# Kernel tuning notes

Hardware: AMD Instinct MI355X
Metric: run time of the kernel (lower is better)

## Reference

```python
import jax, jax.numpy as jnp
import numpy as np
import math

L = 8           # n_layers
DIM = 1024
H = 16          # num_heads
HD = DIM // H   # head_dim
HID = 4096      # mlp hidden
V = 32000       # vocab
B, T = 2, 1024


def setup_inputs() -> dict:
    key = jax.random.key(0)
    ks = jax.random.split(key, 10)
    s = 0.02
    inp = {
        "input_ids": jax.random.randint(ks[0], (B, T), 0, V, dtype=jnp.int32),
        "labels": jax.random.randint(ks[1], (B, T), 0, V, dtype=jnp.int32),
        "Wemb": jax.random.normal(ks[2], (V, DIM), jnp.float32) * s,   # tied embed / lm_head
        "Wq": jax.random.normal(ks[3], (L, DIM, DIM), jnp.float32) * s,
        "Wk": jax.random.normal(ks[4], (L, DIM, DIM), jnp.float32) * s,
        "Wv": jax.random.normal(ks[5], (L, DIM, DIM), jnp.float32) * s,
        "Wo": jax.random.normal(ks[6], (L, DIM, DIM), jnp.float32) * s,
        "Wfc": jax.random.normal(ks[7], (L, DIM, HID), jnp.float32) * s,
        "Wgate": jax.random.normal(ks[8], (L, DIM, HID), jnp.float32) * s,
        "Wproj": jax.random.normal(ks[9], (L, HID, DIM), jnp.float32) * s,
    }
    return inp


def _forward(input_ids, labels, Wemb, Wq, Wk, Wv, Wo, Wfc, Wgate, Wproj):
    b, t = input_ids.shape
    h = Wemb[input_ids]                                   # [B,T,C] embedding lookup
    # causal additive mask: -inf strictly above diagonal
    mask = jnp.triu(jnp.full((t, t), -jnp.inf, dtype=h.dtype), k=1)
    inv_sqrt_L = 1.0 / math.sqrt(L)
    inv_sqrt_hd = 1.0 / math.sqrt(HD)
    inv_sqrt_hid = 1.0 / math.sqrt(HID)

    def block(h, params):
        wq, wk, wv, wo, wfc, wgate, wproj = params
        # attention (explicit QK^T softmax V, as in source)
        q = (h @ wq).reshape(b, t, H, HD)
        k = (h @ wk).reshape(b, t, H, HD)
        v = (h @ wv).reshape(b, t, H, HD)
        scores = jnp.einsum("bqhd,bkhd->bhqk", q, k) * inv_sqrt_hd + mask
        probs = jax.nn.softmax(scores, axis=-1)
        attn = jnp.einsum("bhqk,bkhd->bqhd", probs, v).reshape(b, t, DIM)
        h = h + (attn @ wo) * inv_sqrt_L
        # SwiGLU MLP with 1/sqrt(hidden) scaling
        mlp = (((h @ wfc) * jax.nn.silu(h @ wgate)) * inv_sqrt_hid) @ wproj
        h = h + mlp * inv_sqrt_L
        return h, None

    h, _ = jax.lax.scan(block, h, (Wq, Wk, Wv, Wo, Wfc, Wgate, Wproj))

    logits = h @ Wemb.T                                   # tied lm_head [B,T,V]
    # cross entropy with ignore_index=-1
    lab = labels.reshape(-1)
    valid = lab != -1
    safe = jnp.where(valid, lab, 0)
    logp = jax.nn.log_softmax(logits.reshape(-1, V), axis=-1)
    nll = -jnp.take_along_axis(logp, safe[:, None], axis=-1)[:, 0]
    loss = jnp.sum(jnp.where(valid, nll, 0.0)) / jnp.maximum(jnp.sum(valid), 1)
    return logits, loss


def reference(input_ids, labels, Wemb, Wq, Wk, Wv, Wo, Wfc, Wgate, Wproj):
    return _forward(input_ids, labels, Wemb, Wq, Wk, Wv, Wo, Wfc, Wgate, Wproj)
```

## Files before the change

kernel.cpp:

```cpp
#include <hip/hip_runtime.h>
#include <hip/hip_bf16.h>
#include <math.h>

#define L_LAYERS 8
#define DIM 1024
#define NH 16
#define HD 64
#define HID 4096
#define VOCAB 32000
#define BB 2
#define TT 1024
#define MROWS (BB*TT)

typedef unsigned short u16;
typedef short short8 __attribute__((ext_vector_type(8)));
typedef float f32x4 __attribute__((ext_vector_type(4)));
typedef unsigned short us4 __attribute__((ext_vector_type(4)));
typedef unsigned short us8 __attribute__((ext_vector_type(8)));

__device__ __forceinline__ float bf2f(u16 x){
  union { unsigned int u; float f; } v; v.u = ((unsigned int)x) << 16; return v.f;
}
__device__ __forceinline__ u16 f2bf(float f){
  union { float f; unsigned int u; } v; v.f = f;
  unsigned int r = (v.u + 0x7fffu + ((v.u >> 16) & 1u)) >> 16; return (u16)r;
}

#define AS1 __attribute__((address_space(1)))
#define AS3 __attribute__((address_space(3)))
__device__ __forceinline__ void gld_lds16(const void* g, void* l){
  __builtin_amdgcn_global_load_lds((const AS1 void*)g, (AS3 void*)l, 16, 0, 0);
}

__global__ void k_embed(const int* __restrict__ ids, const float* __restrict__ Wemb,
                        float* __restrict__ h, u16* __restrict__ hb){
  int bt = blockIdx.x; long id = ids[bt];
  const float4* src = (const float4*)(Wemb + id*(long)DIM);
  float4 v = src[threadIdx.x];
  ((float4*)(h + (long)bt*DIM))[threadIdx.x] = v;
  us4 o = { f2bf(v.x), f2bf(v.y), f2bf(v.z), f2bf(v.w) };
  ((us4*)(hb + (long)bt*DIM))[threadIdx.x] = o;
}

__global__ void k_cvt(const float* __restrict__ src, u16* __restrict__ dst, long n){
  long i = ((long)blockIdx.x*256 + threadIdx.x)*8;
  if (i >= n) return;
  float4 a = ((const float4*)(src+i))[0];
  float4 b = ((const float4*)(src+i))[1];
  us4 o0 = { f2bf(a.x), f2bf(a.y), f2bf(a.z), f2bf(a.w) };
  us4 o1 = { f2bf(b.x), f2bf(b.y), f2bf(b.z), f2bf(b.w) };
  ((us4*)(dst+i))[0] = o0; ((us4*)(dst+i))[1] = o1;
}

__global__ void k_cvt_layer(const float* __restrict__ Wq, const float* __restrict__ Wk,
    const float* __restrict__ Wv, const float* __restrict__ Wo,
    const float* __restrict__ Wfc, const float* __restrict__ Wg, const float* __restrict__ Wp,
    u16* __restrict__ qkvT, u16* __restrict__ woT, u16* __restrict__ fgT, u16* __restrict__ projT)
{
  int tile = blockIdx.x;
  const float* src; u16* dst; int R, C, tr, tc;
  long rowmul = 1, rowoff = 0;
  if (tile < 1024){
    int m = tile >> 8, t2 = tile & 255;
    tr = t2 >> 4; tc = t2 & 15; R = 1024; C = 1024;
    src = (m==0)?Wq:(m==1)?Wk:(m==2)?Wv:Wo;
    dst = (m<3)? qkvT + (long)m*1024*1024 : woT;
  } else if (tile < 3072){
    int m = (tile - 1024) >> 10, t2 = (tile - 1024) & 1023;
    tr = t2 >> 6; tc = t2 & 63; R = 1024; C = 4096;
    src = m ? Wg : Wfc; dst = fgT; rowmul = 2; rowoff = m;
  } else {
    int t2 = tile - 3072;
    tr = t2 >> 4; tc = t2 & 15; R = 4096; C = 1024;
    src = Wp; dst = projT;
  }
  __shared__ float ls[64][65];
  int u = threadIdx.x, rr = u & 63, cc = u >> 6;
  const float* sp = src + (long)(tr*64 + rr)*C + tc*64 + cc*16;
  float4 v0 = ((const float4*)sp)[0];
  float4 v1 = ((const float4*)sp)[1];
  float4 v2 = ((const float4*)sp)[2];
  float4 v3 = ((const float4*)sp)[3];
  ls[rr][cc*16+ 0]=v0.x; ls[rr][cc*16+ 1]=v0.y; ls[rr][cc*16+ 2]=v0.z; ls[rr][cc*16+ 3]=v0.w;
  ls[rr][cc*16+ 4]=v1.x; ls[rr][cc*16+ 5]=v1.y; ls[rr][cc*16+ 6]=v1.z; ls[rr][cc*16+ 7]=v1.w;
  ls[rr][cc*16+ 8]=v2.x; ls[rr][cc*16+ 9]=v2.y; ls[rr][cc*16+10]=v2.z; ls[rr][cc*16+11]=v2.w;
  ls[rr][cc*16+12]=v3.x; ls[rr][cc*16+13]=v3.y; ls[rr][cc*16+14]=v3.z; ls[rr][cc*16+15]=v3.w;
  __syncthreads();
  int d  = u >> 2;
  int c4 = u & 3;
  long drow = (long)tc*64 + d;
  u16* dp = dst + (drow*rowmul + rowoff)*R + tr*64;
  #pragma unroll
  for (int g2 = 0; g2 < 2; ++g2){
    int e0 = (c4 + g2*4) * 8;
    us8 o;
    #pragma unroll
    for (int j=0;j<8;j++) o[j] = f2bf(ls[e0+j][d]);
    *((us8*)(dp + e0)) = o;
  }
}

template<int EPI>
__global__ __launch_bounds__(256, 2) void k_gemm(
    const u16* __restrict__ A, long lda,
    const u16* __restrict__ Bt, long ldb,
    void* __restrict__ Cp, long ldc,
    int K, int nMt, float alpha, int ksplit,
    u16* __restrict__ hbout)
{
  __shared__ u16 lsA[128*32];
  __shared__ u16 lsB[128*32];
  int nflat = gridDim.x; int w = blockIdx.x;
  if ((nflat & 7) == 0){ int q = nflat >> 3; w = (w & 7)*q + (w >> 3); }
  int perk = nflat / ksplit;
  int kc = w / perk; int w2 = w - kc*perk;
  int mtile = w2 % nMt, ntile = w2 / nMt;
  const u16* Ab = A + (long)mtile*128*lda + (long)kc*K;
  const u16* Bb = Bt + (long)ntile*128*ldb + (long)kc*K;
  int t = threadIdx.x;
  int wv = t >> 6, ln = t & 63;
  int srow = t >> 2;
  int scol = (t & 3) * 8;
  int fr = ln & 15, kg = ln >> 4;
  int wr = wv >> 1, wc = wv & 1;
  const f32x4 zero = {0.f,0.f,0.f,0.f};
  f32x4 acc[4][4];
  #pragma unroll
  for (int m=0;m<4;m++)
    #pragma unroll
    for (int n=0;n<4;n++) acc[m][n] = zero;
  const u16* ga0 = Ab + (long)srow*lda + scol;
  const u16* ga1 = Ab + (long)(srow+64)*lda + scol;
  const u16* gb0 = Bb + (long)srow*ldb + scol;
  const u16* gb1 = Bb + (long)(srow+64)*ldb + scol;
  u16* la0 = lsA + wv*512;
  u16* la1 = lsA + 2048 + wv*512;
  u16* lb0 = lsB + wv*512;
  u16* lb1 = lsB + 2048 + wv*512;
  for (int k0 = 0; k0 < K; k0 += 32){
    gld_lds16(ga0 + k0, la0);
    gld_lds16(ga1 + k0, la1);
    gld_lds16(gb0 + k0, lb0);
    gld_lds16(gb1 + k0, lb1);
    __syncthreads();
    short8 af[4], bfr[4];
    #pragma unroll
    for (int m=0;m<4;m++) af[m]  = *(const short8*)(lsA + (wr*64 + m*16 + fr)*32 + kg*8);
    #pragma unroll
    for (int n=0;n<4;n++) bfr[n] = *(const short8*)(lsB + (wc*64 + n*16 + fr)*32 + kg*8);
    #pragma unroll
    for (int m=0;m<4;m++)
      #pragma unroll
      for (int n=0;n<4;n++)
        acc[m][n] = __builtin_amdgcn_mfma_f32_16x16x32_bf16(af[m], bfr[n], acc[m][n], 0, 0, 0);
    __syncthreads();
  }
  long row0 = (long)mtile*128 + wr*64 + kg*4;
  int col0 = ntile*128 + wc*64 + fr;
  if constexpr (EPI == 0){
    u16* C = (u16*)Cp;
    #pragma unroll
    for (int m=0;m<4;m++)
      #pragma unroll
      for (int r=0;r<4;r++){
        long row = row0 + m*16 + r;
        #pragma unroll
        for (int n=0;n<4;n++) C[row*ldc + col0 + n*16] = f2bf(acc[m][n][r]);
      }
  } else if constexpr (EPI == 2){
    float* C = (float*)Cp;
    #pragma unroll
    for (int m=0;m<4;m++)
      #pragma unroll
      for (int r=0;r<4;r++){
        long row = row0 + m*16 + r;
        #pragma unroll
        for (int n=0;n<4;n++){
          long idx = row*ldc + col0 + n*16;
          float v = C[idx] + acc[m][n][r]*alpha;
          C[idx] = v;
          hbout[idx] = f2bf(v);
        }
      }
  } else {
    float* C = (float*)Cp + (long)kc*MROWS*ldc;
    #pragma unroll
    for (int m=0;m<4;m++)
      #pragma unroll
      for (int r=0;r<4;r++){
        long row = row0 + m*16 + r;
        #pragma unroll
        for (int n=0;n<4;n++) C[row*ldc + col0 + n*16] = acc[m][n][r];
      }
  }
}

__global__ void k_redK(const float* __restrict__ pK, float* __restrict__ h, u16* __restrict__ hb){
  long idx = ((long)blockIdx.x*256 + threadIdx.x)*4;
  const float aL = 0.35355339059327373f;
  float4 s0 = *(const float4*)(pK + idx);
  float4 s1 = *(const float4*)(pK + idx + (long)MROWS*1024);
  float4 s2 = *(const float4*)(pK + idx + (long)2*MROWS*1024);
  float4 s3 = *(const float4*)(pK + idx + (long)3*MROWS*1024);
  float4 hv = *(const float4*)(h + idx);
  float4 v;
  v.x = hv.x + (s0.x+s1.x+s2.x+s3.x)*aL;
  v.y = hv.y + (s0.y+s1.y+s2.y+s3.y)*aL;
  v.z = hv.z + (s0.z+s1.z+s2.z+s3.z)*aL;
  v.w = hv.w + (s0.w+s1.w+s2.w+s3.w)*aL;
  *(float4*)(h + idx) = v;
  us4 o = { f2bf(v.x), f2bf(v.y), f2bf(v.z), f2bf(v.w) };
  *(us4*)(hb + idx) = o;
}

#define MFMA_(va,vb,vc) __builtin_amdgcn_mfma_f32_16x16x32_bf16(va,vb,vc,0,0,0)
#define RD(slot, row, ku) (*(const short8*)(lds + (slot)*8192 + (row)*64 + ((((ku) ^ ((row)&7)))<<3)))
#define STG(base, ld, h, k0, slot) do{ \
    int u0_ = tid, r0_ = u0_>>3, c0_ = u0_&7; \
    gld_lds16((base) + (long)((h)*128 + r0_)*(ld) + (k0) + ((c0_^(r0_&7))<<3), \
              lds + (slot)*8192 + (wid*64)*8); \
    int u1_ = 512 + tid, r1_ = u1_>>3, c1_ = u1_&7; \
    gld_lds16((base) + (long)((h)*128 + r1_)*(ld) + (k0) + ((c1_^(r1_&7))<<3), \
              lds + (slot)*8192 + (512 + wid*64)*8); \
  }while(0)
#define PHASE(sA, sB, mh, nh, SC, SBASE, SLD, SH, SKOFS, SSLOT, DOWAIT) do{ \
    short8 a00 = RD(sA, wm*64 +  0 + fr, kg); \
    short8 a01 = RD(sA, wm*64 + 16 + fr, kg); \
    short8 a02 = RD(sA, wm*64 + 32 + fr, kg); \
    short8 a03 = RD(sA, wm*64 + 48 + fr, kg); \
    short8 a10 = RD(sA, wm*64 +  0 + fr, 4+kg); \
    short8 a11 = RD(sA, wm*64 + 16 + fr, 4+kg); \
    short8 a12 = RD(sA, wm*64 + 32 + fr, 4+kg); \
    short8 a13 = RD(sA, wm*64 + 48 + fr, 4+kg); \
    short8 b00 = RD(sB, wn*32 +  0 + fr, kg); \
    short8 b01 = RD(sB, wn*32 + 16 + fr, kg); \
    short8 b10 = RD(sB, wn*32 +  0 + fr, 4+kg); \
    short8 b11 = RD(sB, wn*32 + 16 + fr, 4+kg); \
    if (SC) STG(SBASE, SLD, SH, SKOFS, SSLOT); \
    if (DOWAIT){ \
      if (SC) asm volatile("s_waitcnt vmcnt(4)" ::: "memory"); \
      else    asm volatile("s_waitcnt vmcnt(0)" ::: "memory"); \
    } \
    asm volatile("s_barrier" ::: "memory"); \
    __builtin_amdgcn_s_setprio(1); \
    acc[(mh)*4+0][(nh)*2+0] = MFMA_(a00,b00,acc[(mh)*4+0][(nh)*2+0]); \
    acc[(mh)*4+1][(nh)*2+0] = MFMA_(a01,b00,acc[(mh)*4+1][(nh)*2+0]); \
    acc[(mh)*4+2][(nh)*2+0] = MFMA_(a02,b00,acc[(mh)*4+2][(nh)*2+0]); \
    acc[(mh)*4+3][(nh)*2+0] = MFMA_(a03,b00,acc[(mh)*4+3][(nh)*2+0]); \
    acc[(mh)*4+0][(nh)*2+1] = MFMA_(a00,b01,acc[(mh)*4+0][(nh)*2+1]); \
    acc[(mh)*4+1][(nh)*2+1] = MFMA_(a01,b01,acc[(mh)*4+1][(nh)*2+1]); \
    acc[(mh)*4+2][(nh)*2+1] = MFMA_(a02,b01,acc[(mh)*4+2][(nh)*2+1]); \
    acc[(mh)*4+3][(nh)*2+1] = MFMA_(a03,b01,acc[(mh)*4+3][(nh)*2+1]); \
    acc[(mh)*4+0][(nh)*2+0] = MFMA_(a10,b10,acc[(mh)*4+0][(nh)*2+0]); \
    acc[(mh)*4+1][(nh)*2+0] = MFMA_(a11,b10,acc[(mh)*4+1][(nh)*2+0]); \
    acc[(mh)*4+2][(nh)*2+0] = MFMA_(a12,b10,acc[(mh)*4+2][(nh)*2+0]); \
    acc[(mh)*4+3][(nh)*2+0] = MFMA_(a13,b10,acc[(mh)*4+3][(nh)*2+0]); \
    acc[(mh)*4+0][(nh)*2+1] = MFMA_(a10,b11,acc[(mh)*4+0][(nh)*2+1]); \
    acc[(mh)*4+1][(nh)*2+1] = MFMA_(a11,b11,acc[(mh)*4+1][(nh)*2+1]); \
    acc[(mh)*4+2][(nh)*2+1] = MFMA_(a12,b11,acc[(mh)*4+2][(nh)*2+1]); \
    acc[(mh)*4+3][(nh)*2+1] = MFMA_(a13,b11,acc[(mh)*4+3][(nh)*2+1]); \
    __builtin_amdgcn_s_setprio(0); \
    asm volatile("s_barrier" ::: "memory"); \
  }while(0)

template<int EPI>
__global__ __launch_bounds__(512, 1) void k_gemm256(
    const u16* __restrict__ A, long lda,
    const u16* __restrict__ Bt, long ldb,
    void* __restrict__ Cp, long ldc,
    int K, int nMt,
    float2* __restrict__ partials)
{
  __shared__ u16 lds[65536];
  int nwg = gridDim.x; int w = blockIdx.x;
  { int q = nwg >> 3, r8 = nwg & 7; int xcd = w & 7, lw = w >> 3;
    w = (xcd < r8 ? xcd*(q+1) : r8*(q+1) + (xcd-r8)*q) + lw; }
  int mtile = w % nMt, ntile = w / nMt;
  const u16* Abase = A + (long)mtile*256*lda;
  const u16* Bbase = Bt + (long)ntile*256*ldb;
  int tid = threadIdx.x;
  int wid = tid >> 6, ln = tid & 63;
  int wm = wid >> 2, wn = wid & 3;
  int fr = ln & 15, kg = ln >> 4;

  f32x4 acc[8][4];
  #pragma unroll
  for (int a=0;a<8;a++)
    #pragma unroll
    for (int b=0;b<4;b++) acc[a][b] = (f32x4){0.f,0.f,0.f,0.f};

  const int NT = K >> 6;
  STG(Abase, lda, 0, 0, 0);
  STG(Bbase, ldb, 0, 0, 2);
  STG(Abase, lda, 1, 0, 1);
  STG(Bbase, ldb, 1, 0, 3);
  if (NT > 1){
    STG(Abase, lda, 0, 64, 4);
    STG(Bbase, ldb, 1, 64, 7);
    asm volatile("s_waitcnt vmcnt(4)" ::: "memory");
  } else {
    asm volatile("s_waitcnt vmcnt(0)" ::: "memory");
  }
  asm volatile("s_barrier" ::: "memory");

  for (int jt = 0; jt < NT; jt += 2){
    {
      long k1 = ((long)jt+1)<<6, k2 = ((long)jt+2)<<6;
      bool s1 = (jt+1 < NT), s2 = (jt+2 < NT);
      PHASE(0,2,0,0, s1, Abase, lda, 1, k1, 5, 0);
      PHASE(0,3,0,1, s1, Bbase, ldb, 0, k1, 6, 0);
      PHASE(1,3,1,1, s2, Abase, lda, 0, k2, 0, 0);
      PHASE(1,2,1,0, s2, Bbase, ldb, 1, k2, 3, 1);
    }
    if (jt+1 < NT){
      long k1 = ((long)jt+2)<<6, k2 = ((long)jt+3)<<6;
      bool s1 = (jt+2 < NT), s2 = (jt+3 < NT);
      PHASE(4,6,0,0, s1, Abase, lda, 1, k1, 1, 0);
      PHASE(4,7,0,1, s1, Bbase, ldb, 0, k1, 2, 0);
      PHASE(5,7,1,1, s2, Abase, lda, 0, k2, 4, 0);
      PHASE(5,6,1,0, s2, Bbase, ldb, 1, k2, 7, 1);
    }
  }

  if constexpr (EPI == 3){
    u16* act = (u16*)Cp;
    const float sc = 0.015625f;
    #pragma unroll
    for (int a=0;a<8;a++){
      long rowb = (long)mtile*256 + (a>>2)*128 + wm*64 + (a&3)*16 + kg*4;
      #pragma unroll
      for (int r=0;r<4;r++){
        #pragma unroll
        for (int b=0;b<4;b++){
          float v = acc[a][b][r];
          float pv = __shfl_xor(v, 1);
          if (!(fr & 1)){
            int colg = ntile*256 + (b>>1)*128 + wn*32 + (b&1)*16 + fr;
            float g = pv;
            float sl = g / (1.0f + __expf(-g));
            act[(rowb+r)*ldc + (colg>>1)] = f2bf(v * sl * sc);
          }
        }
      }
    }
  } else {
    float* C = (float*)Cp;
    #pragma unroll
    for (int a=0;a<8;a++){
      long rowb = (long)mtile*256 + (a>>2)*128 + wm*64 + (a&3)*16 + kg*4;
      #pragma unroll
      for (int r=0;r<4;r++){
        #pragma unroll
        for (int b=0;b<4;b++){
          int colg = ntile*256 + (b>>1)*128 + wn*32 + (b&1)*16 + fr;
          C[(rowb+r)*ldc + colg] = acc[a][b][r];
        }
      }
    }
    float* pm = (float*)lds;
    float* ps = pm + 1024;
    #pragma unroll
    for (int a=0;a<8;a++)
      #pragma unroll
      for (int r=0;r<4;r++){
        float M = fmaxf(fmaxf(acc[a][0][r],acc[a][1][r]), fmaxf(acc[a][2][r],acc[a][3][r]));
        #pragma unroll
        for (int o=1;o<16;o<<=1) M = fmaxf(M, __shfl_xor(M, o));
        float S = __expf(acc[a][0][r]-M) + __expf(acc[a][1][r]-M)
                + __expf(acc[a][2][r]-M) + __expf(acc[a][3][r]-M);
        #pragma unroll
        for (int o=1;o<16;o<<=1) S += __shfl_xor(S, o);
        if (fr == 0){
          int rl = (a>>2)*128 + wm*64 + (a&3)*16 + kg*4 + r;
          pm[wn*256 + rl] = M; ps[wn*256 + rl] = S;
        }
      }
    __syncthreads();
    if (tid < 256){
      float m0 = pm[tid], m1 = pm[256+tid], m2 = pm[512+tid], m3 = pm[768+tid];
      float M = fmaxf(fmaxf(m0,m1), fmaxf(m2,m3));
      float S = ps[tid]*__expf(m0-M) + ps[256+tid]*__expf(m1-M)
              + ps[512+tid]*__expf(m2-M) + ps[768+tid]*__expf(m3-M);
      partials[((long)mtile*256 + tid)*128 + ntile] = make_float2(M, S);
    }
  }
}

__global__ void k_transpose_v(const u16* __restrict__ qkv, u16* __restrict__ vT){
  int ttile = blockIdx.x; int z = blockIdx.y;
  long b = z >> 4; int hh = z & 15;
  const u16* v = qkv + b*TT*3072 + 2048 + hh*64;
  u16* outp = vT + (long)z*64*TT;
  __shared__ u16 ls[64][65];
  int u = threadIdx.x, rr = u & 63, cc = u >> 6;
  const u16* sp = v + (long)(ttile*64 + rr)*3072 + cc*16;
  us4 a0 = ((const us4*)sp)[0];
  us4 a1 = ((const us4*)sp)[1];
  us4 a2 = ((const us4*)sp)[2];
  us4 a3 = ((const us4*)sp)[3];
  #pragma unroll
  for (int j=0;j<4;j++){ ls[rr][cc*16+j] = a0[j]; ls[rr][cc*16+4+j] = a1[j];
                         ls[rr][cc*16+8+j] = a2[j]; ls[rr][cc*16+12+j] = a3[j]; }
  __syncthreads();
  int d = u & 63;
  #pragma unroll
  for (int g=0; g<4; ++g){
    int tl = cc*16 + g*4;
    int t  = ttile*64 + tl;
    int ut = (t >> 3) & 15;
    int tp = (t & ~127) + (((ut ^ (d & 15)) << 3) | (t & 7));
    us4 o = { ls[tl+0][d], ls[tl+1][d], ls[tl+2][d], ls[tl+3][d] };
    *((us4*)(outp + (long)d*TT + tp)) = o;
  }
}

__global__ __launch_bounds__(128) void k_flash(
    const u16* __restrict__ qkv, const u16* __restrict__ vT, u16* __restrict__ attnb)
{
  __shared__ u16 lsQ[64*64];
  __shared__ u16 lsK[128*64];
  __shared__ u16 lsV[64*128];
  __shared__ u16 lsP[64*128];
  int qt = blockIdx.x; int z = blockIdx.y;
  long bT = (long)(z >> 4) * TT;
  int h64 = (z & 15) * 64;
  int t = threadIdx.x, wv = t >> 6, ln = t & 63;
  int fr = ln & 15, kg = ln >> 4;
  const u16* vbase = vT + (long)z*64*TT;

  #pragma unroll
  for (int p=0; p<4; ++p){
    int r = p*16 + wv*8 + (ln>>3);
    const u16* g = qkv + (bT + qt*64 + r)*3072 + h64 + (((ln&7) ^ (ln>>3))*8);
    gld_lds16(g, lsQ + (p*16 + wv*8)*64);
  }

  f32x4 S[2][8], O[2][4];
  float Mst[2][4], Lst[2][4];
  #pragma unroll
  for (int m=0;m<2;m++){
    #pragma unroll
    for (int n=0;n<4;n++) O[m][n] = (f32x4){0.f,0.f,0.f,0.f};
    #pragma unroll
    for (int r=0;r<4;r++){ Mst[m][r] = -3.0e38f; Lst[m][r] = 0.f; }
  }

  int nk = (qt >> 1) + 1;
  for (int kt = 0; kt < nk; ++kt){
    #pragma unroll
    for (int p=0; p<8; ++p){
      int r = p*16 + wv*8 + (ln>>3);
      const u16* g = qkv + (bT + kt*128 + r)*3072 + 1024 + h64 + (((ln&7) ^ (ln>>3))*8);
      gld_lds16(g, lsK + (p*16 + wv*8)*64);
    }
    #pragma unroll
    for (int p=0; p<8; ++p){
      int d = p*8 + wv*4 + (ln>>4);
      const u16* g = vbase + (long)d*TT + kt*128 + (ln&15)*8;
      gld_lds16(g, lsV + (p*8 + wv*4)*128);
    }
    __syncthreads();

    #pragma unroll
    for (int m=0;m<2;m++)
      #pragma unroll
      for (int n=0;n<8;n++) S[m][n] = (f32x4){0.f,0.f,0.f,0.f};
    #pragma unroll
    for (int ks=0; ks<2; ++ks){
      int un = ((ks*4 + kg) ^ (fr & 7)) * 8;
      short8 a0 = *(const short8*)(lsQ + (wv*32 +      fr)*64 + un);
      short8 a1 = *(const short8*)(lsQ + (wv*32 + 16 + fr)*64 + un);
      #pragma unroll
      for (int n=0;n<8;n++){
        short8 bb = *(const short8*)(lsK + (n*16 + fr)*64 + un);
        S[0][n] = __builtin_amdgcn_mfma_f32_16x16x32_bf16(a0, bb, S[0][n], 0,0,0);
        S[1][n] = __builtin_amdgcn_mfma_f32_16x16x32_bf16(a1, bb, S[1][n], 0,0,0);
      }
    }

    #pragma unroll
    for (int m=0;m<2;m++){
      #pragma unroll
      for (int r=0;r<4;r++){
        int rloc = wv*32 + m*16 + kg*4 + r;
        int row_g = qt*64 + rloc;
        float x[8]; float mx = -3.0e38f;
        #pragma unroll
        for (int n=0;n<8;n++){
          int col_g = kt*128 + n*16 + fr;
          x[n] = (col_g <= row_g) ? S[m][n][r]*0.125f : -3.0e38f;
          mx = fmaxf(mx, x[n]);
        }
        #pragma unroll
        for (int o=1;o<16;o<<=1) mx = fmaxf(mx, __shfl_xor(mx, o));
        float Mnew = fmaxf(Mst[m][r], mx);
        float corr = __expf(Mst[m][r] - Mnew);
        Mst[m][r] = Mnew;
        float s = 0.f;
        #pragma unroll
        for (int n=0;n<8;n++){
          float p = __expf(x[n] - Mnew);
          s += p;
          int col = n*16 + fr;
          int col2 = ((((col>>3) ^ (rloc & 15)) << 3) | (col & 7));
          lsP[rloc*128 + col2] = f2bf(p);
        }
        #pragma unroll
        for (int o=1;o<16;o<<=1) s += __shfl_xor(s, o);
        Lst[m][r] = Lst[m][r]*corr + s;
        #pragma unroll
        for (int n=0;n<4;n++) O[m][n][r] *= corr;
      }
    }

    #pragma unroll
    for (int ks=0; ks<4; ++ks){
      int up = ((ks*4 + kg) ^ fr) * 8;
      short8 p0 = *(const short8*)(lsP + (wv*32 +      fr)*128 + up);
      short8 p1 = *(const short8*)(lsP + (wv*32 + 16 + fr)*128 + up);
      #pragma unroll
      for (int n=0;n<4;n++){
        short8 vb = *(const short8*)(lsV + (n*16 + fr)*128 + up);
        O[0][n] = __builtin_amdgcn_mfma_f32_16x16x32_bf16(p0, vb, O[0][n], 0,0,0);
        O[1][n] = __builtin_amdgcn_mfma_f32_16x16x32_bf16(p1, vb, O[1][n], 0,0,0);
      }
    }
    __syncthreads();
  }

  #pragma unroll
  for (int m=0;m<2;m++)
    #pragma unroll
    for (int r=0;r<4;r++){
      float inv = 1.0f / Lst[m][r];
      long row = bT + qt*64 + wv*32 + m*16 + kg*4 + r;
      #pragma unroll
      for (int n=0;n<4;n++)
        attnb[row*1024 + h64 + n*16 + fr] = f2bf(O[m][n][r]*inv);
    }
}

__global__ void k_nll2(const float2* __restrict__ part, const float* __restrict__ logits,
                       const int* __restrict__ labels, float* __restrict__ nll){
  int row = blockIdx.x; int ln = threadIdx.x;
  const float2* pr = part + (long)row*128;
  float m = -3.0e38f, s = 0.f;
  for (int j = ln; j < 125; j += 64){
    float2 p = pr[j];
    float M = fmaxf(m, p.x);
    s = s*__expf(m - M) + p.y*__expf(p.x - M);
    m = M;
  }
  #pragma unroll
  for (int o=32;o;o>>=1){
    float om = __shfl_xor(m, o), os = __shfl_xor(s, o);
    float M = fmaxf(m, om);
    s = s*__expf(m - M) + os*__expf(om - M);
    m = M;
  }
  if (ln == 0){
    int lab = labels[row];
    float lse = m + __logf(s);
    nll[row] = (lab != -1) ? (lse - logits[(long)row*VOCAB + lab]) : 0.f;
  }
}

__global__ void k_loss(const float* __restrict__ nll, const int* __restrict__ labels,
                       float* __restrict__ out){
  int tid = threadIdx.x;
  int wv = tid >> 6;
  float s = 0.f; float c = 0.f;
  for (int i = tid; i < MROWS; i += 256){
    s += nll[i];
    c += (labels[i] != -1) ? 1.f : 0.f;
  }
  #pragma unroll
  for (int o=32;o;o>>=1){ s += __shfl_xor(s, o); c += __shfl_xor(c, o); }
  __shared__ float rsm[4], rc[4];
  if ((tid & 63) == 0){ rsm[wv] = s; rc[wv] = c; }
  __syncthreads();
  if (tid == 0){
    s = rsm[0]+rsm[1]+rsm[2]+rsm[3];
    c = rc[0]+rc[1]+rc[2]+rc[3];
    out[(long)MROWS*VOCAB] = s / fmaxf(c, 1.f);
  }
}

extern "C" void kernel_launch(void* const* d_in, const int* in_sizes, int n_in,
                              void* d_out, int out_size, void* d_ws, size_t ws_size,
                              hipStream_t stream)
{
  (void)in_sizes; (void)n_in; (void)out_size; (void)ws_size;
  const int*   ids    = (const int*)d_in[0];
  const int*   labels = (const int*)d_in[1];
  const float* Wemb   = (const float*)d_in[2];
  const float* Wq     = (const float*)d_in[3];
  const float* Wk     = (const float*)d_in[4];
  const float* Wv     = (const float*)d_in[5];
  const float* Wo     = (const float*)d_in[6];
  const float* Wfc    = (const float*)d_in[7];
  const float* Wg     = (const float*)d_in[8];
  const float* Wp     = (const float*)d_in[9];
  float* logits = (float*)d_out;

  char* ws = (char*)d_ws;
  size_t off = 0;
  auto alloc = [&](size_t bytes){ void* p = ws + off; off += (bytes + 255) & ~(size_t)255; return p; };
  u16*    wembBf = (u16*)alloc((size_t)VOCAB*DIM*2);
  float*  h      = (float*)alloc((size_t)MROWS*DIM*4);
  u16*    hb     = (u16*)alloc((size_t)MROWS*DIM*2);
  u16*    qkvT   = (u16*)alloc((size_t)3*DIM*DIM*2);
  u16*    woT    = (u16*)alloc((size_t)DIM*DIM*2);
  u16*    fgT    = (u16*)alloc((size_t)2*HID*DIM*2);
  u16*    projT  = (u16*)alloc((size_t)DIM*HID*2);
  u16*    qkv    = (u16*)alloc((size_t)MROWS*3*DIM*2);
  u16*    vT     = (u16*)alloc((size_t)BB*NH*64*TT*2);
  u16*    attnb  = (u16*)alloc((size_t)MROWS*DIM*2);
  u16*    act    = (u16*)alloc((size_t)MROWS*HID*2);
  float*  pK     = (float*)alloc((size_t)4*MROWS*DIM*4);
  float2* parts  = (float2*)alloc((size_t)MROWS*128*8);
  float*  nllb   = (float*)alloc((size_t)MROWS*4);

  dim3 blk(256,1,1);
  dim3 blk512(512,1,1);
  const float aL = 0.35355339059327373f;

  k_cvt<<<dim3(16000,1,1),blk,0,stream>>>(Wemb, wembBf, (long)VOCAB*DIM);
  k_embed<<<dim3(MROWS,1,1),blk,0,stream>>>(ids, Wemb, h, hb);

  for (int l = 0; l < L_LAYERS; ++l){
    k_cvt_layer<<<dim3(4096,1,1),blk,0,stream>>>(
        Wq + (size_t)l*DIM*DIM, Wk + (size_t)l*DIM*DIM, Wv + (size_t)l*DIM*DIM, Wo + (size_t)l*DIM*DIM,
        Wfc + (size_t)l*DIM*HID, Wg + (size_t)l*DIM*HID, Wp + (size_t)l*HID*DIM,
        qkvT, woT, fgT, projT);
    k_gemm<0><<<dim3(384,1,1),blk,0,stream>>>(hb,1024, qkvT,1024, qkv,3072,
        1024,16,1.f,1, nullptr);
    k_transpose_v<<<dim3(16,32,1),blk,0,stream>>>(qkv, vT);
    k_flash<<<dim3(16,32,1),dim3(128,1,1),0,stream>>>(qkv, vT, attnb);
    k_gemm<2><<<dim3(128,1,1),blk,0,stream>>>(attnb,1024, woT,1024, h,1024,
        1024,16,aL,1, hb);
    k_gemm256<3><<<dim3(256,1,1),blk512,0,stream>>>(hb,1024, fgT,1024, act,4096,
        1024,8, nullptr);
    k_gemm<5><<<dim3(512,1,1),blk,0,stream>>>(act,4096, projT,4096, pK,1024,
        1024,16,1.f,4, nullptr);
    k_redK<<<dim3(2048,1,1),blk,0,stream>>>(pK, h, hb);
  }
  k_gemm256<4><<<dim3(1000,1,1),blk512,0,stream>>>(hb,1024, wembBf,1024, logits,32000,
      1024,8, parts);
  k_nll2<<<dim3(MROWS,1,1),dim3(64,1,1),0,stream>>>(parts, logits, labels, nllb);
  k_loss<<<dim3(1,1,1),blk,0,stream>>>(nllb, labels, logits);
}
```

Baseline: 1.973 ms.

## Restructure 256-tile GEMM LDS addressing and reorder flash-attention causal block schedule

```diff
diff --git a/kernel.cpp b/kernel.cpp
--- a/kernel.cpp
+++ b/kernel.cpp
@@ -214,34 +214,41 @@
 }
 
 #define MFMA_(va,vb,vc) __builtin_amdgcn_mfma_f32_16x16x32_bf16(va,vb,vc,0,0,0)
-#define RD(slot, row, ku) (*(const short8*)(lds + (slot)*8192 + (row)*64 + ((((ku) ^ ((row)&7)))<<3)))
-#define STG(base, ld, h, k0, slot) do{ \
-    int u0_ = tid, r0_ = u0_>>3, c0_ = u0_&7; \
-    gld_lds16((base) + (long)((h)*128 + r0_)*(ld) + (k0) + ((c0_^(r0_&7))<<3), \
-              lds + (slot)*8192 + (wid*64)*8); \
-    int u1_ = 512 + tid, r1_ = u1_>>3, c1_ = u1_&7; \
-    gld_lds16((base) + (long)((h)*128 + r1_)*(ld) + (k0) + ((c1_^(r1_&7))<<3), \
-              lds + (slot)*8192 + (512 + wid*64)*8); \
+#define RDX(sOff, rbase, i, kuo) (*(const short8*)((const u16*)lds + (sOff) + (rbase) + (i)*1024 + (kuo)))
+#define STGX(isB, half, dbf, kt) do{ \
+    u16* d_ = (u16*)lds + (((dbf)*4 + ((isB)? 2+(half) : (half)))*8192) + (wid<<9); \
+    if (!(isB)){ \
+      const u16* s_ = Abase + (long)((half)*64)*lda + aSrcOff + ((long)(kt)<<6); \
+      gld_lds16(s_, d_); \
+      gld_lds16(s_ + 128*lda, d_ + 4096); \
+    } else { \
+      const u16* s_ = Bbase + (long)((half)*32)*ldb + bSrcOff + ((long)(kt)<<6); \
+      gld_lds16(s_, d_); \
+      gld_lds16(s_ + 128*ldb, d_ + 4096); \
+    } \
   }while(0)
-#define PHASE(sA, sB, mh, nh, SC, SBASE, SLD, SH, SKOFS, SSLOT, DOWAIT) do{ \
-    short8 a00 = RD(sA, wm*64 +  0 + fr, kg); \
-    short8 a01 = RD(sA, wm*64 + 16 + fr, kg); \
-    short8 a02 = RD(sA, wm*64 + 32 + fr, kg); \
-    short8 a03 = RD(sA, wm*64 + 48 + fr, kg); \
-    short8 a10 = RD(sA, wm*64 +  0 + fr, 4+kg); \
-    short8 a11 = RD(sA, wm*64 + 16 + fr, 4+kg); \
-    short8 a12 = RD(sA, wm*64 + 32 + fr, 4+kg); \
-    short8 a13 = RD(sA, wm*64 + 48 + fr, 4+kg); \
-    short8 b00 = RD(sB, wn*32 +  0 + fr, kg); \
-    short8 b01 = RD(sB, wn*32 + 16 + fr, kg); \
-    short8 b10 = RD(sB, wn*32 +  0 + fr, 4+kg); \
-    short8 b11 = RD(sB, wn*32 + 16 + fr, 4+kg); \
-    if (SC) STG(SBASE, SLD, SH, SKOFS, SSLOT); \
-    if (DOWAIT){ \
-      if (SC) asm volatile("s_waitcnt vmcnt(4)" ::: "memory"); \
-      else    asm volatile("s_waitcnt vmcnt(0)" ::: "memory"); \
+#define PH(dbf, mh, nh, DOSTG, SisB, Shalf, Sdbf, Skt, WKIND) do{ \
+    const int sA_ = ((dbf)*4 + (mh))*8192; \
+    const int sB_ = ((dbf)*4 + 2 + (nh))*8192; \
+    short8 a00 = RDX(sA_, aRdBase, 0, kuo0); \
+    short8 a01 = RDX(sA_, aRdBase, 1, kuo0); \
+    short8 a02 = RDX(sA_, aRdBase, 2, kuo0); \
+    short8 a03 = RDX(sA_, aRdBase, 3, kuo0); \
+    short8 b00 = RDX(sB_, bRdBase, 0, kuo0); \
+    short8 b01 = RDX(sB_, bRdBase, 1, kuo0); \
+    short8 a10 = RDX(sA_, aRdBase, 0, kuo1); \
+    short8 a11 = RDX(sA_, aRdBase, 1, kuo1); \
+    short8 a12 = RDX(sA_, aRdBase, 2, kuo1); \
+    short8 a13 = RDX(sA_, aRdBase, 3, kuo1); \
+    short8 b10 = RDX(sB_, bRdBase, 0, kuo1); \
+    short8 b11 = RDX(sB_, bRdBase, 1, kuo1); \
+    if (DOSTG) STGX(SisB, Shalf, Sdbf, Skt); \
+    if (WKIND){ \
+      if (DOSTG) asm volatile("s_waitcnt vmcnt(4)" ::: "memory"); \
+      else       asm volatile("s_waitcnt vmcnt(0)" ::: "memory"); \
     } \
-    asm volatile("s_barrier" ::: "memory"); \
+    __builtin_amdgcn_s_barrier(); \
+    asm volatile("s_waitcnt lgkmcnt(0)"); \
     __builtin_amdgcn_s_setprio(1); \
     acc[(mh)*4+0][(nh)*2+0] = MFMA_(a00,b00,acc[(mh)*4+0][(nh)*2+0]); \
     acc[(mh)*4+1][(nh)*2+0] = MFMA_(a01,b00,acc[(mh)*4+1][(nh)*2+0]); \
@@ -260,7 +267,7 @@
     acc[(mh)*4+2][(nh)*2+1] = MFMA_(a12,b11,acc[(mh)*4+2][(nh)*2+1]); \
     acc[(mh)*4+3][(nh)*2+1] = MFMA_(a13,b11,acc[(mh)*4+3][(nh)*2+1]); \
     __builtin_amdgcn_s_setprio(0); \
-    asm volatile("s_barrier" ::: "memory"); \
+    __builtin_amdgcn_s_barrier(); \
   }while(0)
 
 template<int EPI>
@@ -282,6 +289,16 @@
   int wid = tid >> 6, ln = tid & 63;
   int wm = wid >> 2, wn = wid & 3;
   int fr = ln & 15, kg = ln >> 4;
+  int fr7 = fr & 7;
+  int kuo0 = ((kg     ) ^ fr7) << 3;
+  int kuo1 = ((kg + 4 ) ^ fr7) << 3;
+  int aRdBase = (wm*64 + fr)*64;
+  int bRdBase = (wn*32 + fr)*64;
+  int trow = tid >> 3;
+  int tu   = tid & 7;
+  long ku8 = (long)((tu ^ (trow & 7)) << 3);
+  long aSrcOff = (long)trow*lda + ku8;
+  long bSrcOff = (long)(((trow >> 5) << 6) + (trow & 31))*ldb + ku8;
 
   f32x4 acc[8][4];
   #pragma unroll
@@ -290,36 +307,30 @@
     for (int b=0;b<4;b++) acc[a][b] = (f32x4){0.f,0.f,0.f,0.f};
 
   const int NT = K >> 6;
-  STG(Abase, lda, 0, 0, 0);
-  STG(Bbase, ldb, 0, 0, 2);
-  STG(Abase, lda, 1, 0, 1);
-  STG(Bbase, ldb, 1, 0, 3);
+  STGX(0,0,0, 0);
+  STGX(1,0,0, 0);
+  STGX(0,1,0, 0);
+  STGX(1,1,0, 0);
   if (NT > 1){
-    STG(Abase, lda, 0, 64, 4);
-    STG(Bbase, ldb, 1, 64, 7);
+    STGX(0,0,1, 1);
+    STGX(1,1,1, 1);
     asm volatile("s_waitcnt vmcnt(4)" ::: "memory");
   } else {
     asm volatile("s_waitcnt vmcnt(0)" ::: "memory");
   }
-  asm volatile("s_barrier" ::: "memory");
-
+  __builtin_amdgcn_s_barrier();
+
+  #pragma unroll 1
   for (int jt = 0; jt < NT; jt += 2){
-    {
-      long k1 = ((long)jt+1)<<6, k2 = ((long)jt+2)<<6;
-      bool s1 = (jt+1 < NT), s2 = (jt+2 < NT);
-      PHASE(0,2,0,0, s1, Abase, lda, 1, k1, 5, 0);
-      PHASE(0,3,0,1, s1, Bbase, ldb, 0, k1, 6, 0);
-      PHASE(1,3,1,1, s2, Abase, lda, 0, k2, 0, 0);
-      PHASE(1,2,1,0, s2, Bbase, ldb, 1, k2, 3, 1);
-    }
-    if (jt+1 < NT){
-      long k1 = ((long)jt+2)<<6, k2 = ((long)jt+3)<<6;
-      bool s1 = (jt+2 < NT), s2 = (jt+3 < NT);
-      PHASE(4,6,0,0, s1, Abase, lda, 1, k1, 1, 0);
-      PHASE(4,7,0,1, s1, Bbase, ldb, 0, k1, 2, 0);
-      PHASE(5,7,1,1, s2, Abase, lda, 0, k2, 4, 0);
-      PHASE(5,6,1,0, s2, Bbase, ldb, 1, k2, 7, 1);
-    }
+    int s2 = (jt+2 < NT), s3 = (jt+3 < NT);
+    PH(0, 0,0, 1,  0,1,1, jt+1, 0);
+    PH(0, 0,1, 1,  1,0,1, jt+1, 0);
+    PH(0, 1,1, s2, 0,0,0, jt+2, 0);
+    PH(0, 1,0, s2, 1,1,0, jt+2, 1);
+    PH(1, 0,0, s2, 0,1,0, jt+2, 0);
+    PH(1, 0,1, s2, 1,0,0, jt+2, 0);
+    PH(1, 1,1, s3, 0,0,1, jt+3, 0);
+    PH(1, 1,0, s3, 1,1,1, jt+3, 1);
   }
 
   if constexpr (EPI == 3){
@@ -327,7 +338,7 @@
     const float sc = 0.015625f;
     #pragma unroll
     for (int a=0;a<8;a++){
-      long rowb = (long)mtile*256 + (a>>2)*128 + wm*64 + (a&3)*16 + kg*4;
+      long rowb = (long)mtile*256 + wm*128 + (a>>2)*64 + (a&3)*16 + kg*4;
       #pragma unroll
       for (int r=0;r<4;r++){
         #pragma unroll
@@ -335,7 +346,7 @@
           float v = acc[a][b][r];
           float pv = __shfl_xor(v, 1);
           if (!(fr & 1)){
-            int colg = ntile*256 + (b>>1)*128 + wn*32 + (b&1)*16 + fr;
+            int colg = ntile*256 + wn*64 + (b>>1)*32 + (b&1)*16 + fr;
             float g = pv;
             float sl = g / (1.0f + __expf(-g));
             act[(rowb+r)*ldc + (colg>>1)] = f2bf(v * sl * sc);
@@ -347,16 +358,17 @@
     float* C = (float*)Cp;
     #pragma unroll
     for (int a=0;a<8;a++){
-      long rowb = (long)mtile*256 + (a>>2)*128 + wm*64 + (a&3)*16 + kg*4;
+      long rowb = (long)mtile*256 + wm*128 + (a>>2)*64 + (a&3)*16 + kg*4;
       #pragma unroll
       for (int r=0;r<4;r++){
         #pragma unroll
         for (int b=0;b<4;b++){
-          int colg = ntile*256 + (b>>1)*128 + wn*32 + (b&1)*16 + fr;
+          int colg = ntile*256 + wn*64 + (b>>1)*32 + (b&1)*16 + fr;
           C[(rowb+r)*ldc + colg] = acc[a][b][r];
         }
       }
     }
+    __syncthreads();
     float* pm = (float*)lds;
     float* ps = pm + 1024;
     #pragma unroll
@@ -371,7 +383,7 @@
         #pragma unroll
         for (int o=1;o<16;o<<=1) S += __shfl_xor(S, o);
         if (fr == 0){
-          int rl = (a>>2)*128 + wm*64 + (a&3)*16 + kg*4 + r;
+          int rl = wm*128 + (a>>2)*64 + (a&3)*16 + kg*4 + r;
           pm[wn*256 + rl] = M; ps[wn*256 + rl] = S;
         }
       }
@@ -421,7 +433,9 @@
   __shared__ u16 lsK[128*64];
   __shared__ u16 lsV[64*128];
   __shared__ u16 lsP[64*128];
-  int qt = blockIdx.x; int z = blockIdx.y;
+  int id = blockIdx.x;
+  int wq = id >> 5, z = id & 31;
+  int qt = (wq < 8) ? wq : 23 - wq;
   long bT = (long)(z >> 4) * TT;
   int h64 = (z & 15) * 64;
   int t = threadIdx.x, wv = t >> 6, ln = t & 63;
@@ -636,7 +650,7 @@
     k_gemm<0><<<dim3(384,1,1),blk,0,stream>>>(hb,1024, qkvT,1024, qkv,3072,
         1024,16,1.f,1, nullptr);
     k_transpose_v<<<dim3(16,32,1),blk,0,stream>>>(qkv, vT);
-    k_flash<<<dim3(16,32,1),dim3(128,1,1),0,stream>>>(qkv, vT, attnb);
+    k_flash<<<dim3(512,1,1),dim3(128,1,1),0,stream>>>(qkv, vT, attnb);
     k_gemm<2><<<dim3(128,1,1),blk,0,stream>>>(attnb,1024, woT,1024, h,1024,
         1024,16,aL,1, hb);
     k_gemm256<3><<<dim3(256,1,1),blk512,0,stream>>>(hb,1024, fgT,1024, act,4096,
```

Result: faster. 1.928 ms (-2.3%).
